# Performance work log

Measured on AMD Instinct MI355X. Metric: run time of the kernel, lower is better.

The kernel has to match this reference:

```python
import jax, jax.numpy as jnp
import numpy as np

MAX_RADIUS = 10.0
NUM_BASIS = 3
H = 100
C = 32  # dim(Rs_hidden) with scalar-only irreps
LEAKY_SLOPE = 0.01

def swish(v):
    return v * jax.nn.sigmoid(v)


def setup_inputs() -> dict:
    key = jax.random.key(0)
    ks = jax.random.split(key, 10)
    B, N = 4, 256
    x = jax.random.normal(ks[0], (B, N, C), dtype=jnp.float32)
    xyz = jax.random.normal(ks[1], (B, N, 3), dtype=jnp.float32) * 3.0
    mask = jax.random.randint(ks[2], (B, N), 0, 2).astype(jnp.int64)
    # radial MLP (GaussianRadialModel): basis(3) -> h(100) -> C*C path weights
    rw1 = jax.random.normal(ks[3], (NUM_BASIS, H), dtype=jnp.float32) / np.sqrt(NUM_BASIS)
    rw2 = jax.random.normal(ks[4], (H, C * C), dtype=jnp.float32) / np.sqrt(H)
    # fc3: Linear(C, C); fc2: Linear(C, 1)
    fc3_w = jax.random.normal(ks[5], (C, C), dtype=jnp.float32) / np.sqrt(C)
    fc3_b = jax.random.normal(ks[6], (C,), dtype=jnp.float32) * 0.01
    fc2_w = jax.random.normal(ks[7], (C, 1), dtype=jnp.float32) / np.sqrt(C)
    fc2_b = jax.random.normal(ks[8], (1,), dtype=jnp.float32) * 0.01
    return {"x": x, "xyz": xyz, "mask": mask, "rw1": rw1, "rw2": rw2,
            "fc3_w": fc3_w, "fc3_b": fc3_b, "fc2_w": fc2_w, "fc2_b": fc2_b}


def _normalize(v, eps=1e-6):
    mean = jnp.mean(v, axis=-1, keepdims=True)
    std = jnp.std(v, axis=-1, keepdims=True, ddof=1)  # torch std is unbiased
    return (v - mean) / (std + eps)


def reference(x, xyz, mask, rw1, rw2, fc3_w, fc3_b, fc2_w, fc2_b):
    B, N, Cc = x.shape
    # --- fc1: e3nn point convolution with Gaussian radial kernel (l=0 paths) ---
    diff = xyz[:, :, None, :] - xyz[:, None, :, :]            # [B,N,N,3]
    r = jnp.sqrt(jnp.sum(diff * diff, axis=-1) + 1e-12)       # [B,N,N]
    spacing = MAX_RADIUS / NUM_BASIS
    centers = jnp.linspace(0.0, MAX_RADIUS, NUM_BASIS, dtype=jnp.float32)
    gamma = 1.0 / spacing
    basis = jnp.exp(-gamma * (r[..., None] - centers) ** 2)   # [B,N,N,3]
    hid = swish(jnp.einsum('zabk,kh->zabh', basis, rw1))      # [B,N,N,H]
    K = jnp.einsum('zabh,hf->zabf', hid, rw2).reshape(B, N, N, Cc, Cc)  # per-pair kernel
    out = jnp.einsum('zabij,zbj->zai', K, x) / jnp.sqrt(jnp.float32(N))  # [B,N,C]
    # --- Norm(Rs_hidden): per-irrep L2 norm; for l=0 channels this is |x| ---
    out = jnp.abs(out)
    # --- mask + sum pool over points ---
    out = jnp.where(mask[..., None] == 0, 0.0, out)
    pooled = jnp.sum(out, axis=1)                             # [B,C]
    pooled = _normalize(pooled)
    # --- MLP head: leaky_relu(fc3) -> fc2 -> flatten ---
    h1 = pooled @ fc3_w + fc3_b
    h1 = jnp.where(h1 >= 0, h1, LEAKY_SLOPE * h1)
    y = h1 @ fc2_w + fc2_b                                    # [B,1]
    return y.reshape(-1)
```

## Files before the change

kernel.cpp:

```cpp
#include <hip/hip_runtime.h>
#include <math.h>

#define GAMMA 0.3f
#define WSTR  1608

typedef __bf16 bf16x8 __attribute__((ext_vector_type(8)));
typedef __bf16 bf16x4 __attribute__((ext_vector_type(4)));
typedef float  f32x4  __attribute__((ext_vector_type(4)));

__global__ __launch_bounds__(512) void k2_fused(const float* __restrict__ x,
                                                const float* __restrict__ xyz,
                                                const float* __restrict__ rw1,
                                                const float* __restrict__ rw2,
                                                float* __restrict__ part) {
    extern __shared__ char smem[];
    __bf16* Wlds = (__bf16*)smem;
    float*  rw1s = (float*)(smem + 32 * WSTR * 2);
    float (*red)[2][16][17] = (float(*)[2][16][17])(smem + 32 * WSTR * 2 + 1216);

    int bid = blockIdx.x;
    int ac = bid & 3;
    int bc = (bid >> 2) & 15;
    int z  = bid >> 6;
    int t  = threadIdx.x;
    int w  = t >> 6;
    int wa = w >> 1, wk = w & 1;
    int l  = t & 63;
    int l16 = l & 15, lg = l >> 4;

    for (int e = t; e < 300; e += 512) rw1s[e] = rw1[e];

    int a_glob = ac * 64 + wa * 16 + l16;
    float ax = xyz[(z * 256 + a_glob) * 3 + 0];
    float ay = xyz[(z * 256 + a_glob) * 3 + 1];
    float az = xyz[(z * 256 + a_glob) * 3 + 2];
    float bas[4][3];
    #pragma unroll
    for (int e = 0; e < 4; ++e) {
        int b_glob = bc * 16 + lg * 4 + e;
        float dx = xyz[(z * 256 + b_glob) * 3 + 0] - ax;
        float dy = xyz[(z * 256 + b_glob) * 3 + 1] - ay;
        float dz = xyz[(z * 256 + b_glob) * 3 + 2] - az;
        float r  = sqrtf(dx * dx + dy * dy + dz * dz + 1e-12f);
        float r5 = r - 5.f, r10 = r - 10.f;
        bas[e][0] = __expf(-GAMMA * r * r);
        bas[e][1] = __expf(-GAMMA * r5 * r5);
        bas[e][2] = __expf(-GAMMA * r10 * r10);
    }

    bf16x8 xa;
    {
        int row = (z * 256 + bc * 16 + l16) * 32;
        float4 v0 = *(const float4*)(x + row + lg * 4);
        float4 v1 = *(const float4*)(x + row + lg * 4 + 16);
        xa[0] = (__bf16)v0.x; xa[1] = (__bf16)v0.y; xa[2] = (__bf16)v0.z; xa[3] = (__bf16)v0.w;
        xa[4] = (__bf16)v1.x; xa[5] = (__bf16)v1.y; xa[6] = (__bf16)v1.z; xa[7] = (__bf16)v1.w;
    }
    for (int q = 0; q < 25; ++q) {
        int nt = w * 25 + q;
        int h  = nt >> 1;
        int icol = ((nt & 1) << 4) + l16;
        const float* rp = rw2 + h * 1024 + icol * 32 + lg * 4;
        float4 r0 = *(const float4*)rp;
        float4 r1 = *(const float4*)(rp + 16);
        bf16x8 rb;
        rb[0] = (__bf16)r0.x; rb[1] = (__bf16)r0.y; rb[2] = (__bf16)r0.z; rb[3] = (__bf16)r0.w;
        rb[4] = (__bf16)r1.x; rb[5] = (__bf16)r1.y; rb[6] = (__bf16)r1.z; rb[7] = (__bf16)r1.w;
        f32x4 d = {0.f, 0.f, 0.f, 0.f};
        d = __builtin_amdgcn_mfma_f32_16x16x32_bf16(xa, rb, d, 0, 0, 0);
        bf16x4 pk;
        pk[0] = (__bf16)d[0]; pk[1] = (__bf16)d[1]; pk[2] = (__bf16)d[2]; pk[3] = (__bf16)d[3];
        *(bf16x4*)&Wlds[icol * WSTR + h * 16 + lg * 4] = pk;
    }
    __syncthreads();

    f32x4 acc0 = {0.f, 0.f, 0.f, 0.f};
    f32x4 acc1 = {0.f, 0.f, 0.f, 0.f};
    for (int ks = 0; ks < 25; ++ks) {
        int hp = wk * 25 + ks;
        int h0 = 2 * hp, h1 = h0 + 1;
        float u00 = rw1s[h0],       u01 = rw1s[h1];
        float u10 = rw1s[100 + h0], u11 = rw1s[100 + h1];
        float u20 = rw1s[200 + h0], u21 = rw1s[200 + h1];
        bf16x8 af;
        #pragma unroll
        for (int e = 0; e < 4; ++e) {
            float p0 = bas[e][0] * u00 + bas[e][1] * u10 + bas[e][2] * u20;
            float p1 = bas[e][0] * u01 + bas[e][1] * u11 + bas[e][2] * u21;
            float s0 = p0 * __builtin_amdgcn_rcpf(1.f + __expf(-p0));
            float s1 = p1 * __builtin_amdgcn_rcpf(1.f + __expf(-p1));
            af[e]     = (__bf16)s0;
            af[e + 4] = (__bf16)s1;
        }
        int kb = hp * 32 + lg * 4;
        const __bf16* w0 = &Wlds[l16 * WSTR + kb];
        const __bf16* w1 = w0 + 16 * WSTR;
        bf16x4 b0l = *(const bf16x4*)w0, b0h = *(const bf16x4*)(w0 + 16);
        bf16x4 b1l = *(const bf16x4*)w1, b1h = *(const bf16x4*)(w1 + 16);
        bf16x8 bf0 = __builtin_shufflevector(b0l, b0h, 0, 1, 2, 3, 4, 5, 6, 7);
        bf16x8 bf1 = __builtin_shufflevector(b1l, b1h, 0, 1, 2, 3, 4, 5, 6, 7);
        acc0 = __builtin_amdgcn_mfma_f32_16x16x32_bf16(af, bf0, acc0, 0, 0, 0);
        acc1 = __builtin_amdgcn_mfma_f32_16x16x32_bf16(af, bf1, acc1, 0, 0, 0);
    }

    if (wk == 1) {
        #pragma unroll
        for (int r = 0; r < 4; ++r) {
            red[wa][0][lg * 4 + r][l16] = acc0[r];
            red[wa][1][lg * 4 + r][l16] = acc1[r];
        }
    }
    __syncthreads();
    if (wk == 0) {
        #pragma unroll
        for (int r = 0; r < 4; ++r) {
            float v0 = acc0[r] + red[wa][0][lg * 4 + r][l16];
            float v1 = acc1[r] + red[wa][1][lg * 4 + r][l16];
            int a = ac * 64 + wa * 16 + lg * 4 + r;
            size_t base = ((size_t)(z * 16 + bc) * 256 + a) * 32;
            part[base + l16]      = v0;
            part[base + 16 + l16] = v1;
        }
    }
}

__global__ __launch_bounds__(256) void k3a_reduce(const float* __restrict__ part,
                                                  const int* __restrict__ mask,
                                                  float* __restrict__ pooled_part) {
    int blk = blockIdx.x;
    int z = blk >> 6, ag = blk & 63;
    int t = threadIdx.x;
    int i = t & 31;
    int qg = (t >> 5) & 1;
    int a_loc = t >> 6;
    int a = ag * 4 + a_loc;
    const float* base = part + ((size_t)z * 16 * 256 + (size_t)a) * 32 + i;
    float s = 0.f;
    for (int q = qg; q < 16; q += 2)
        s += base[(size_t)q * 8192];
    __shared__ float buf[4][2][32];
    buf[a_loc][qg][i] = s;
    __syncthreads();
    if (t < 128) {
        int al = t >> 5, ii = t & 31;
        float v = buf[al][0][ii] + buf[al][1][ii];
        float sc = (mask[z * 256 + ag * 4 + al] != 0) ? 0.0625f : 0.f;
        buf[al][0][ii] = fabsf(v) * sc;
    }
    __syncthreads();
    if (t < 32) {
        float v = buf[0][0][t] + buf[1][0][t] + buf[2][0][t] + buf[3][0][t];
        pooled_part[(z * 64 + ag) * 32 + t] = v;
    }
}

__global__ __launch_bounds__(128) void k3b_final(const float* __restrict__ pooled_part,
                                                 const float* __restrict__ fc3_w,
                                                 const float* __restrict__ fc3_b,
                                                 const float* __restrict__ fc2_w,
                                                 const float* __restrict__ fc2_b,
                                                 float* __restrict__ out) {
    int t = threadIdx.x;
    int z = t >> 5, i = t & 31;
    float s = 0.f;
    for (int ag = 0; ag < 64; ++ag) s += pooled_part[(z * 64 + ag) * 32 + i];
    float sm = s;
    #pragma unroll
    for (int off = 16; off; off >>= 1) sm += __shfl_xor(sm, off, 32);
    float mean = sm * (1.f / 32.f);
    float d = s - mean;
    float ss = d * d;
    #pragma unroll
    for (int off = 16; off; off >>= 1) ss += __shfl_xor(ss, off, 32);
    float stdv = sqrtf(ss * (1.f / 31.f));
    float nv = d / (stdv + 1e-6f);
    __shared__ float pn[4][32];
    pn[z][i] = nv;
    __syncthreads();
    float h1 = fc3_b[i];
    #pragma unroll
    for (int j = 0; j < 32; ++j) h1 += pn[z][j] * fc3_w[j * 32 + i];
    h1 = (h1 >= 0.f) ? h1 : 0.01f * h1;
    float y = h1 * fc2_w[i];
    #pragma unroll
    for (int off = 16; off; off >>= 1) y += __shfl_xor(y, off, 32);
    if (i == 0) out[z] = y + fc2_b[0];
}

extern "C" void kernel_launch(void* const* d_in, const int* in_sizes, int n_in,
                              void* d_out, int out_size, void* d_ws, size_t ws_size,
                              hipStream_t stream) {
    const float* x    = (const float*)d_in[0];
    const float* xyz  = (const float*)d_in[1];
    const int*   mask = (const int*)d_in[2];
    const float* rw1  = (const float*)d_in[3];
    const float* rw2  = (const float*)d_in[4];
    const float* fc3w = (const float*)d_in[5];
    const float* fc3b = (const float*)d_in[6];
    const float* fc2w = (const float*)d_in[7];
    const float* fc2b = (const float*)d_in[8];
    float* out = (float*)d_out;

    float* part        = (float*)d_ws;
    float* pooled_part = (float*)((char*)d_ws + 2097152);

    const int LDS_BYTES = 32 * WSTR * 2 + 1216 + 8704;

    hipLaunchKernelGGL(k2_fused,   dim3(256), dim3(512), LDS_BYTES, stream, x, xyz, rw1, rw2, part);
    hipLaunchKernelGGL(k3a_reduce, dim3(256), dim3(256), 0, stream, part, mask, pooled_part);
    hipLaunchKernelGGL(k3b_final,  dim3(1),   dim3(128), 0, stream, pooled_part, fc3w, fc3b, fc2w, fc2b, out);
}
```

Baseline: 34.92 us.

## Split hidden dim across blocks, halve LDS, fuse final head via atomic counter

Each k2 block now covers 128 target points and half of the 100 hidden units, instead of 64 points and all hidden units split across warp pairs. This halves the LDS weight tile, removes the intra-block reduction and its barrier, and uses a k-interleaved layout so each B fragment is one 16-byte LDS read. The partial buffer doubles to 32 slices, which are reduced in the next kernel. The separate single-block head kernel is folded into the reduce kernel using a last-block atomic counter, which adds a memset launch in exchange for one fewer kernel launch.

```diff
diff --git a/kernel.cpp b/kernel.cpp
--- a/kernel.cpp
+++ b/kernel.cpp
@@ -2,7 +2,7 @@
 #include <math.h>
 
 #define GAMMA 0.3f
-#define WSTR  1608
+#define WSTR2 808
 
 typedef __bf16 bf16x8 __attribute__((ext_vector_type(8)));
 typedef __bf16 bf16x4 __attribute__((ext_vector_type(4)));
@@ -15,22 +15,21 @@
                                                 float* __restrict__ part) {
     extern __shared__ char smem[];
     __bf16* Wlds = (__bf16*)smem;
-    float*  rw1s = (float*)(smem + 32 * WSTR * 2);
-    float (*red)[2][16][17] = (float(*)[2][16][17])(smem + 32 * WSTR * 2 + 1216);
+    float*  rw1s = (float*)(smem + 32 * WSTR2 * 2);
 
     int bid = blockIdx.x;
-    int ac = bid & 3;
+    int ah = bid & 1;
+    int hh = (bid >> 1) & 1;
     int bc = (bid >> 2) & 15;
     int z  = bid >> 6;
     int t  = threadIdx.x;
     int w  = t >> 6;
-    int wa = w >> 1, wk = w & 1;
     int l  = t & 63;
     int l16 = l & 15, lg = l >> 4;
 
     for (int e = t; e < 300; e += 512) rw1s[e] = rw1[e];
 
-    int a_glob = ac * 64 + wa * 16 + l16;
+    int a_glob = ah * 128 + w * 16 + l16;
     float ax = xyz[(z * 256 + a_glob) * 3 + 0];
     float ay = xyz[(z * 256 + a_glob) * 3 + 1];
     float az = xyz[(z * 256 + a_glob) * 3 + 2];
@@ -56,77 +55,74 @@
         xa[0] = (__bf16)v0.x; xa[1] = (__bf16)v0.y; xa[2] = (__bf16)v0.z; xa[3] = (__bf16)v0.w;
         xa[4] = (__bf16)v1.x; xa[5] = (__bf16)v1.y; xa[6] = (__bf16)v1.z; xa[7] = (__bf16)v1.w;
     }
-    for (int q = 0; q < 25; ++q) {
-        int nt = w * 25 + q;
-        int h  = nt >> 1;
-        int icol = ((nt & 1) << 4) + l16;
-        const float* rp = rw2 + h * 1024 + icol * 32 + lg * 4;
-        float4 r0 = *(const float4*)rp;
-        float4 r1 = *(const float4*)(rp + 16);
-        bf16x8 rb;
-        rb[0] = (__bf16)r0.x; rb[1] = (__bf16)r0.y; rb[2] = (__bf16)r0.z; rb[3] = (__bf16)r0.w;
-        rb[4] = (__bf16)r1.x; rb[5] = (__bf16)r1.y; rb[6] = (__bf16)r1.z; rb[7] = (__bf16)r1.w;
-        f32x4 d = {0.f, 0.f, 0.f, 0.f};
-        d = __builtin_amdgcn_mfma_f32_16x16x32_bf16(xa, rb, d, 0, 0, 0);
-        bf16x4 pk;
-        pk[0] = (__bf16)d[0]; pk[1] = (__bf16)d[1]; pk[2] = (__bf16)d[2]; pk[3] = (__bf16)d[3];
-        *(bf16x4*)&Wlds[icol * WSTR + h * 16 + lg * 4] = pk;
+    for (int q = 0; q < 13; ++q) {
+        int nt = q * 8 + w;
+        if (nt < 100) {
+            int h_loc = nt >> 1;
+            int h = hh * 50 + h_loc;
+            int hp_loc = h_loc >> 1, hpar = h_loc & 1;
+            int icol = ((nt & 1) << 4) + l16;
+            const float* rp = rw2 + h * 1024 + icol * 32 + lg * 4;
+            float4 r0 = *(const float4*)rp;
+            float4 r1 = *(const float4*)(rp + 16);
+            bf16x8 rb;
+            rb[0] = (__bf16)r0.x; rb[1] = (__bf16)r0.y; rb[2] = (__bf16)r0.z; rb[3] = (__bf16)r0.w;
+            rb[4] = (__bf16)r1.x; rb[5] = (__bf16)r1.y; rb[6] = (__bf16)r1.z; rb[7] = (__bf16)r1.w;
+            f32x4 d = {0.f, 0.f, 0.f, 0.f};
+            d = __builtin_amdgcn_mfma_f32_16x16x32_bf16(xa, rb, d, 0, 0, 0);
+            bf16x4 pk;
+            pk[0] = (__bf16)d[0]; pk[1] = (__bf16)d[1]; pk[2] = (__bf16)d[2]; pk[3] = (__bf16)d[3];
+            *(bf16x4*)&Wlds[icol * WSTR2 + hp_loc * 32 + lg * 8 + hpar * 4] = pk;
+        }
     }
     __syncthreads();
 
     f32x4 acc0 = {0.f, 0.f, 0.f, 0.f};
     f32x4 acc1 = {0.f, 0.f, 0.f, 0.f};
     for (int ks = 0; ks < 25; ++ks) {
-        int hp = wk * 25 + ks;
-        int h0 = 2 * hp, h1 = h0 + 1;
-        float u00 = rw1s[h0],       u01 = rw1s[h1];
-        float u10 = rw1s[100 + h0], u11 = rw1s[100 + h1];
-        float u20 = rw1s[200 + h0], u21 = rw1s[200 + h1];
+        int h0 = hh * 50 + 2 * ks;
+        float2 u0 = *(const float2*)&rw1s[h0];
+        float2 u1 = *(const float2*)&rw1s[100 + h0];
+        float2 u2 = *(const float2*)&rw1s[200 + h0];
         bf16x8 af;
         #pragma unroll
         for (int e = 0; e < 4; ++e) {
-            float p0 = bas[e][0] * u00 + bas[e][1] * u10 + bas[e][2] * u20;
-            float p1 = bas[e][0] * u01 + bas[e][1] * u11 + bas[e][2] * u21;
+            float p0 = bas[e][0] * u0.x + bas[e][1] * u1.x + bas[e][2] * u2.x;
+            float p1 = bas[e][0] * u0.y + bas[e][1] * u1.y + bas[e][2] * u2.y;
             float s0 = p0 * __builtin_amdgcn_rcpf(1.f + __expf(-p0));
             float s1 = p1 * __builtin_amdgcn_rcpf(1.f + __expf(-p1));
             af[e]     = (__bf16)s0;
             af[e + 4] = (__bf16)s1;
         }
-        int kb = hp * 32 + lg * 4;
-        const __bf16* w0 = &Wlds[l16 * WSTR + kb];
-        const __bf16* w1 = w0 + 16 * WSTR;
-        bf16x4 b0l = *(const bf16x4*)w0, b0h = *(const bf16x4*)(w0 + 16);
-        bf16x4 b1l = *(const bf16x4*)w1, b1h = *(const bf16x4*)(w1 + 16);
-        bf16x8 bf0 = __builtin_shufflevector(b0l, b0h, 0, 1, 2, 3, 4, 5, 6, 7);
-        bf16x8 bf1 = __builtin_shufflevector(b1l, b1h, 0, 1, 2, 3, 4, 5, 6, 7);
+        int kb = ks * 32 + lg * 8;
+        bf16x8 bf0 = *(const bf16x8*)&Wlds[l16 * WSTR2 + kb];
+        bf16x8 bf1 = *(const bf16x8*)&Wlds[(16 + l16) * WSTR2 + kb];
         acc0 = __builtin_amdgcn_mfma_f32_16x16x32_bf16(af, bf0, acc0, 0, 0, 0);
         acc1 = __builtin_amdgcn_mfma_f32_16x16x32_bf16(af, bf1, acc1, 0, 0, 0);
     }
 
-    if (wk == 1) {
-        #pragma unroll
-        for (int r = 0; r < 4; ++r) {
-            red[wa][0][lg * 4 + r][l16] = acc0[r];
-            red[wa][1][lg * 4 + r][l16] = acc1[r];
-        }
-    }
-    __syncthreads();
-    if (wk == 0) {
-        #pragma unroll
-        for (int r = 0; r < 4; ++r) {
-            float v0 = acc0[r] + red[wa][0][lg * 4 + r][l16];
-            float v1 = acc1[r] + red[wa][1][lg * 4 + r][l16];
-            int a = ac * 64 + wa * 16 + lg * 4 + r;
-            size_t base = ((size_t)(z * 16 + bc) * 256 + a) * 32;
-            part[base + l16]      = v0;
-            part[base + 16 + l16] = v1;
-        }
+    int qc = bc * 2 + hh;
+    #pragma unroll
+    for (int r = 0; r < 4; ++r) {
+        int a = ah * 128 + w * 16 + lg * 4 + r;
+        size_t base = ((size_t)(z * 32 + qc) * 256 + a) * 32;
+        part[base + l16]      = acc0[r];
+        part[base + 16 + l16] = acc1[r];
     }
 }
 
-__global__ __launch_bounds__(256) void k3a_reduce(const float* __restrict__ part,
-                                                  const int* __restrict__ mask,
-                                                  float* __restrict__ pooled_part) {
+__global__ __launch_bounds__(256) void k3_fused(const float* __restrict__ part,
+                                                const int* __restrict__ mask,
+                                                const float* __restrict__ fc3_w,
+                                                const float* __restrict__ fc3_b,
+                                                const float* __restrict__ fc2_w,
+                                                const float* __restrict__ fc2_b,
+                                                float* __restrict__ pooled_part,
+                                                unsigned* __restrict__ cnt,
+                                                float* __restrict__ out) {
+    __shared__ float buf[4][2][32];
+    __shared__ float pn[32];
+    __shared__ int isLastS;
     int blk = blockIdx.x;
     int z = blk >> 6, ag = blk & 63;
     int t = threadIdx.x;
@@ -134,11 +130,10 @@
     int qg = (t >> 5) & 1;
     int a_loc = t >> 6;
     int a = ag * 4 + a_loc;
-    const float* base = part + ((size_t)z * 16 * 256 + (size_t)a) * 32 + i;
+    const float* base = part + ((size_t)z * 32 * 256 + (size_t)a) * 32 + i;
     float s = 0.f;
-    for (int q = qg; q < 16; q += 2)
+    for (int q = qg; q < 32; q += 2)
         s += base[(size_t)q * 8192];
-    __shared__ float buf[4][2][32];
     buf[a_loc][qg][i] = s;
     __syncthreads();
     if (t < 128) {
@@ -152,39 +147,42 @@
         float v = buf[0][0][t] + buf[1][0][t] + buf[2][0][t] + buf[3][0][t];
         pooled_part[(z * 64 + ag) * 32 + t] = v;
     }
-}
-
-__global__ __launch_bounds__(128) void k3b_final(const float* __restrict__ pooled_part,
-                                                 const float* __restrict__ fc3_w,
-                                                 const float* __restrict__ fc3_b,
-                                                 const float* __restrict__ fc2_w,
-                                                 const float* __restrict__ fc2_b,
-                                                 float* __restrict__ out) {
-    int t = threadIdx.x;
-    int z = t >> 5, i = t & 31;
-    float s = 0.f;
-    for (int ag = 0; ag < 64; ++ag) s += pooled_part[(z * 64 + ag) * 32 + i];
-    float sm = s;
-    #pragma unroll
-    for (int off = 16; off; off >>= 1) sm += __shfl_xor(sm, off, 32);
-    float mean = sm * (1.f / 32.f);
-    float d = s - mean;
-    float ss = d * d;
-    #pragma unroll
-    for (int off = 16; off; off >>= 1) ss += __shfl_xor(ss, off, 32);
-    float stdv = sqrtf(ss * (1.f / 31.f));
-    float nv = d / (stdv + 1e-6f);
-    __shared__ float pn[4][32];
-    pn[z][i] = nv;
-    __syncthreads();
-    float h1 = fc3_b[i];
-    #pragma unroll
-    for (int j = 0; j < 32; ++j) h1 += pn[z][j] * fc3_w[j * 32 + i];
-    h1 = (h1 >= 0.f) ? h1 : 0.01f * h1;
-    float y = h1 * fc2_w[i];
-    #pragma unroll
-    for (int off = 16; off; off >>= 1) y += __shfl_xor(y, off, 32);
-    if (i == 0) out[z] = y + fc2_b[0];
+
+    __threadfence();
+    __syncthreads();
+    if (t == 0) {
+        unsigned old = atomicAdd(&cnt[z], 1u);
+        isLastS = (old == 63u);
+    }
+    __syncthreads();
+    if (!isLastS) return;
+    __threadfence();
+
+    if (t < 32) {
+        float p = 0.f;
+        for (int g = 0; g < 64; ++g) p += pooled_part[(z * 64 + g) * 32 + t];
+        float sm = p;
+        #pragma unroll
+        for (int off = 16; off; off >>= 1) sm += __shfl_xor(sm, off, 32);
+        float mean = sm * (1.f / 32.f);
+        float d = p - mean;
+        float ss = d * d;
+        #pragma unroll
+        for (int off = 16; off; off >>= 1) ss += __shfl_xor(ss, off, 32);
+        float stdv = sqrtf(ss * (1.f / 31.f));
+        pn[t] = d / (stdv + 1e-6f);
+    }
+    __syncthreads();
+    if (t < 32) {
+        float h1 = fc3_b[t];
+        #pragma unroll
+        for (int j = 0; j < 32; ++j) h1 += pn[j] * fc3_w[j * 32 + t];
+        h1 = (h1 >= 0.f) ? h1 : 0.01f * h1;
+        float y = h1 * fc2_w[t];
+        #pragma unroll
+        for (int off = 16; off; off >>= 1) y += __shfl_xor(y, off, 32);
+        if (t == 0) out[z] = y + fc2_b[0];
+    }
 }
 
 extern "C" void kernel_launch(void* const* d_in, const int* in_sizes, int n_in,
@@ -201,12 +199,15 @@
     const float* fc2b = (const float*)d_in[8];
     float* out = (float*)d_out;
 
-    float* part        = (float*)d_ws;
-    float* pooled_part = (float*)((char*)d_ws + 2097152);
-
-    const int LDS_BYTES = 32 * WSTR * 2 + 1216 + 8704;
-
-    hipLaunchKernelGGL(k2_fused,   dim3(256), dim3(512), LDS_BYTES, stream, x, xyz, rw1, rw2, part);
-    hipLaunchKernelGGL(k3a_reduce, dim3(256), dim3(256), 0, stream, part, mask, pooled_part);
-    hipLaunchKernelGGL(k3b_final,  dim3(1),   dim3(128), 0, stream, pooled_part, fc3w, fc3b, fc2w, fc2b, out);
+    float*    part        = (float*)d_ws;
+    float*    pooled_part = (float*)((char*)d_ws + 4194304);
+    unsigned* cnt         = (unsigned*)((char*)d_ws + 4227072);
+
+    const int LDS_BYTES = 32 * WSTR2 * 2 + 1216;
+
+    hipMemsetAsync(cnt, 0, 16, stream);
+    hipLaunchKernelGGL(k2_fused, dim3(256), dim3(512), LDS_BYTES, stream,
+                       x, xyz, rw1, rw2, part);
+    hipLaunchKernelGGL(k3_fused, dim3(256), dim3(256), 0, stream,
+                       part, mask, fc3w, fc3b, fc2w, fc2b, pooled_part, cnt, out);
 }
```

Measured after the change: 53.73 us. +53.9%, slower.
